# Kernel optimization log

Measured on AMD Instinct MI355X. Metric: run time of the kernel, lower is better.

Reference implementation:

```python
import jax, jax.numpy as jnp
import numpy as np

EPS = 1e-8           # torch.cosine_similarity norm clamp
TEMPERATURE = 0.2    # from __init__ default


def setup_inputs() -> dict:
    key = jax.random.key(0)
    k1, k2, k3 = jax.random.split(key, 3)
    B, C, D = 16384, 1000, 2048  # batch, num_classes, embedding_size
    querys = jax.random.normal(k1, (B, D), dtype=jnp.float32)
    prototype = jax.random.normal(k2, (C, D), dtype=jnp.float32)
    fc_w = jax.random.normal(k3, (C, D), dtype=jnp.float32) * 0.02
    fc_b = jnp.zeros((C,), dtype=jnp.float32)
    return {"querys": querys, "prototype": prototype, "fc_w": fc_w, "fc_b": fc_b}


def _memory_prototype_attention(querys, prototype):
    # cosine similarity of every query against every prototype, fused as one GEMM
    qn = jnp.maximum(jnp.linalg.norm(querys, axis=1, keepdims=True), EPS)      # [B,1]
    pn = jnp.maximum(jnp.linalg.norm(prototype, axis=1, keepdims=True), EPS)   # [C,1]
    cos = jnp.einsum('bd,cd->bc', querys / qn, prototype / pn)                 # [B,C]
    attn = jax.nn.softmax(cos / TEMPERATURE, axis=1)                           # [B,C]
    enhanced = jnp.einsum('bc,cd->bd', attn, prototype)                        # [B,D]
    # original skips rows where the raw score sum is exactly zero
    nonzero = (jnp.sum(cos, axis=1, keepdims=True) != 0)
    return jnp.where(nonzero, enhanced, jnp.zeros_like(enhanced))


def reference(querys, prototype, fc_w, fc_b):
    embedding = querys  # post-avgpool features in the original forward
    enhanced = jax.lax.stop_gradient(_memory_prototype_attention(querys, prototype))
    x = querys + enhanced
    logits = x @ fc_w.T + fc_b  # [B, num_classes]
    return (logits, embedding)
```

## Files before the change

### kernel.cpp

```cpp
#include <hip/hip_runtime.h>
#include <hip/hip_bf16.h>
#include <cstdint>
#include <math.h>

typedef __attribute__((ext_vector_type(8))) __bf16 bfx8;
typedef __attribute__((ext_vector_type(4))) __bf16 bfx4;
typedef __attribute__((ext_vector_type(4))) float f32x4;

#define EPSN 1e-8f
#define SM_SCALE 7.2134752044448170f

__device__ __forceinline__ void gload_lds16(const void* g, void* l) {
    __builtin_amdgcn_global_load_lds(
        (__attribute__((address_space(1))) void*)g,
        (__attribute__((address_space(3))) void*)l,
        16, 0, 0);
}

__global__ __launch_bounds__(256) void qnorm_kernel(
    const float* __restrict__ q, __bf16* __restrict__ qbf,
    float* __restrict__ emb, int D) {
    const int tid = threadIdx.x;
    const size_t roff = (size_t)blockIdx.x * D;
    const float4* qr = (const float4*)(q + roff);
    float4* er = (float4*)(emb + roff);
    const int PASS = D >> 10;
    float4 v[4];
    float ss = 0.f;
    for (int p = 0; p < PASS; ++p) {
        v[p] = qr[p * 256 + tid];
        ss += v[p].x * v[p].x + v[p].y * v[p].y + v[p].z * v[p].z + v[p].w * v[p].w;
    }
    for (int o = 32; o; o >>= 1) ss += __shfl_xor(ss, o);
    __shared__ float sred[4];
    if ((tid & 63) == 0) sred[tid >> 6] = ss;
    __syncthreads();
    float tot = sred[0] + sred[1] + sred[2] + sred[3];
    float inv = 1.f / fmaxf(sqrtf(tot), EPSN);
    for (int p = 0; p < PASS; ++p) {
        er[p * 256 + tid] = v[p];
        bfx4 o4 = {(__bf16)(v[p].x * inv), (__bf16)(v[p].y * inv),
                   (__bf16)(v[p].z * inv), (__bf16)(v[p].w * inv)};
        *(bfx4*)(qbf + roff + (size_t)(p * 256 + tid) * 4) = o4;
    }
}

__global__ __launch_bounds__(256) void pnorm_kernel(
    const float* __restrict__ P, const float* __restrict__ W,
    __bf16* __restrict__ Pn, __bf16* __restrict__ Wb,
    int C, int D) {
    const int c = blockIdx.x;
    const int tid = threadIdx.x;
    const int PASS = D >> 10;
    if (c >= C) {
        bfx4 z = {(__bf16)0.f, (__bf16)0.f, (__bf16)0.f, (__bf16)0.f};
        for (int p = 0; p < PASS; ++p) {
            size_t e = (size_t)c * D + (size_t)(p * 256 + tid) * 4;
            *(bfx4*)(Pn + e) = z;
            *(bfx4*)(Wb + e) = z;
        }
        return;
    }
    const float4* pr = (const float4*)(P + (size_t)c * D);
    float4 v[4];
    float ss = 0.f;
    for (int p = 0; p < PASS; ++p) {
        v[p] = pr[p * 256 + tid];
        ss += v[p].x * v[p].x + v[p].y * v[p].y + v[p].z * v[p].z + v[p].w * v[p].w;
    }
    for (int o = 32; o; o >>= 1) ss += __shfl_xor(ss, o);
    __shared__ float sred[4];
    if ((tid & 63) == 0) sred[tid >> 6] = ss;
    __syncthreads();
    float tot = sred[0] + sred[1] + sred[2] + sred[3];
    float inv = 1.f / fmaxf(sqrtf(tot), EPSN);
    const float4* wr_ = (const float4*)(W + (size_t)c * D);
    for (int p = 0; p < PASS; ++p) {
        size_t e = (size_t)c * D + (size_t)(p * 256 + tid) * 4;
        bfx4 o4 = {(__bf16)(v[p].x * inv), (__bf16)(v[p].y * inv),
                   (__bf16)(v[p].z * inv), (__bf16)(v[p].w * inv)};
        *(bfx4*)(Pn + e) = o4;
        float4 wv = wr_[p * 256 + tid];
        bfx4 w4 = {(__bf16)wv.x, (__bf16)wv.y, (__bf16)wv.z, (__bf16)wv.w};
        *(bfx4*)(Wb + e) = w4;
    }
}

__global__ __launch_bounds__(256) void ptrans_kernel(
    const float* __restrict__ P, __bf16* __restrict__ PT,
    int C, int D, int CP) {
    __shared__ float t[64][65];
    const int d0 = blockIdx.x * 64;
    const int c0 = blockIdx.y * 64;
    const int tid = threadIdx.x;
#pragma unroll
    for (int it = 0; it < 16; ++it) {
        int idx = it * 256 + tid;
        int r = idx >> 6;
        int cc = idx & 63;
        float v = 0.f;
        if (c0 + r < C) v = P[(size_t)(c0 + r) * D + d0 + cc];
        t[r][cc] = v;
    }
    __syncthreads();
#pragma unroll
    for (int it = 0; it < 16; ++it) {
        int idx = it * 256 + tid;
        int dd = idx >> 6;
        int c = idx & 63;
        PT[(size_t)(d0 + dd) * CP + c0 + c] = (__bf16)t[c][dd];
    }
}

__global__ __launch_bounds__(256) void softmax_kernel(
    __bf16* __restrict__ S, int C, int CP) {
    const int tid = threadIdx.x;
    __bf16* row = S + (size_t)blockIdx.x * CP;
    bfx4 v4 = *(const bfx4*)(row + tid * 4);
    const int base = tid * 4;
    float v[4];
    float mx = -INFINITY, rs = 0.f;
#pragma unroll
    for (int j = 0; j < 4; ++j) {
        v[j] = (float)v4[j];
        if (base + j < C) { mx = fmaxf(mx, v[j]); rs += v[j]; }
    }
    for (int o = 32; o; o >>= 1) {
        mx = fmaxf(mx, __shfl_xor(mx, o));
        rs += __shfl_xor(rs, o);
    }
    __shared__ float smx[4], srs[4], sps[4];
    if ((tid & 63) == 0) { smx[tid >> 6] = mx; srs[tid >> 6] = rs; }
    __syncthreads();
    mx = fmaxf(fmaxf(smx[0], smx[1]), fmaxf(smx[2], smx[3]));
    rs = srs[0] + srs[1] + srs[2] + srs[3];
    float p[4], ps = 0.f;
#pragma unroll
    for (int j = 0; j < 4; ++j) {
        p[j] = (base + j < C) ? exp2f((v[j] - mx) * SM_SCALE) : 0.f;
        ps += p[j];
    }
    for (int o = 32; o; o >>= 1) ps += __shfl_xor(ps, o);
    if ((tid & 63) == 0) sps[tid >> 6] = ps;
    __syncthreads();
    ps = sps[0] + sps[1] + sps[2] + sps[3];
    float inv = (rs != 0.f) ? 1.f / ps : 0.f;
    bfx4 o4 = {(__bf16)(p[0] * inv), (__bf16)(p[1] * inv),
               (__bf16)(p[2] * inv), (__bf16)(p[3] * inv)};
    *(bfx4*)(row + tid * 4) = o4;
}

template <int MODE>
__global__ __launch_bounds__(512, 2) void gemm8p(
    const __bf16* __restrict__ A, const __bf16* __restrict__ B_,
    int K, int NT, int nbxl, int nwg,
    void* __restrict__ out, const float* __restrict__ aux, int ldout) {
    __shared__ __bf16 lds[65536];

    const int tid = threadIdx.x;
    const int lane = tid & 63, wid = tid >> 6;
    const int wr = wid >> 2, wc = wid & 3;
    const int fr = lane & 15, fq = lane >> 4;
    const int wr4 = wr * 4, wc2 = wc * 2;
    const int frs = fr * 32 + ((fq * 8) ^ ((fr & 8) << 1));

    const int nbx = 1 << nbxl;
    const int lin = blockIdx.y * nbx + blockIdx.x;
    const int swz = (lin & 7) * (nwg >> 3) + (lin >> 3);
    const int bm0 = (swz >> nbxl) * 256;
    const int bn0 = (swz & (nbx - 1)) * 256;

    int row0, col0, row1, col1;
    {
        int Le = tid * 8;
        int st = Le >> 9, w = Le & 511;
        row0 = (st >> 1) * 16 + (w >> 5);
        col0 = (st & 1) * 32 + ((w & 31) ^ ((w >> 4) & 16));
        Le = tid * 8 + 4096;
        st = Le >> 9; w = Le & 511;
        row1 = (st >> 1) * 16 + (w >> 5);
        col1 = (st & 1) * 32 + ((w & 31) ^ ((w >> 4) & 16));
    }
    const __bf16* Ap = A + (size_t)bm0 * K;
    const __bf16* Bp = B_ + (size_t)bn0 * K;

    auto STAGE = [&](int s) {
        const int t = s >> 2, h = s & 3;
        const int kt = t << 6;
        const int be = ((t & 1) << 14) + ((h >> 1) << 13);
        const __bf16* src = (h & 1) ? Bp : Ap;
        src += (size_t)((h >> 1) * 128) * K + kt;
        __bf16* d = (h & 1) ? (lds + 32768 + be) : (lds + be);
        gload_lds16(src + (size_t)row0 * K + col0, d + tid * 8);
        gload_lds16(src + (size_t)row1 * K + col1, d + tid * 8 + 4096);
    };

    f32x4 acc[4][4][2] = {};

#define PHASE(Q, T, SS, WMODE) do {                                            \
    const int qm_ = (Q) >> 1, qn_ = (Q) & 1;                                   \
    const int bufe_ = ((T) & 1) << 14;                                         \
    bfx8 af_[4][2], bb_[2][2];                                                 \
    _Pragma("unroll") for (int m_ = 0; m_ < 4; ++m_)                           \
      _Pragma("unroll") for (int ks_ = 0; ks_ < 2; ++ks_)                      \
        af_[m_][ks_] = *(const bfx8*)&lds[bufe_ +                              \
            (((qm_ * 8 + wr4 + m_) * 2 + ks_) << 9) + frs];                    \
    _Pragma("unroll") for (int n_ = 0; n_ < 2; ++n_)                           \
      _Pragma("unroll") for (int ks_ = 0; ks_ < 2; ++ks_)                      \
        bb_[n_][ks_] = *(const bfx8*)&lds[32768 + bufe_ +                      \
            (((qn_ * 8 + wc2 + n_) * 2 + ks_) << 9) + frs];                    \
    if ((SS) >= 0) STAGE(SS);                                                  \
    __builtin_amdgcn_s_barrier();                                              \
    asm volatile("s_waitcnt lgkmcnt(0)" ::: "memory");                         \
    __builtin_amdgcn_s_setprio(1);                                             \
    _Pragma("unroll") for (int ks_ = 0; ks_ < 2; ++ks_)                        \
      _Pragma("unroll") for (int m_ = 0; m_ < 4; ++m_)                         \
        _Pragma("unroll") for (int n_ = 0; n_ < 2; ++n_)                       \
          acc[Q][m_][n_] = __builtin_amdgcn_mfma_f32_16x16x32_bf16(            \
              af_[m_][ks_], bb_[n_][ks_], acc[Q][m_][n_], 0, 0, 0);            \
    __builtin_amdgcn_s_setprio(0);                                             \
    if ((WMODE) == 1) asm volatile("s_waitcnt vmcnt(4)" ::: "memory");         \
    else if ((WMODE) == 2) asm volatile("s_waitcnt vmcnt(0)" ::: "memory");    \
    __builtin_amdgcn_s_barrier();                                              \
} while (0)

#pragma unroll
    for (int s = 0; s < 6; ++s) STAGE(s);
    asm volatile("s_waitcnt vmcnt(4)" ::: "memory");
    __builtin_amdgcn_s_barrier();

    int T = 0;
    for (; T <= NT - 3; ++T) {
        PHASE(0, T, 4 * T + 6, 0);
        PHASE(1, T, 4 * T + 7, 0);
        PHASE(2, T, 4 * T + 8, 0);
        PHASE(3, T, 4 * T + 9, 1);
    }
    PHASE(0, T, 4 * T + 6, 0);
    PHASE(1, T, 4 * T + 7, 0);
    PHASE(2, T, -1, 0);
    PHASE(3, T, -1, 2);
    ++T;
    PHASE(0, T, -1, 0);
    PHASE(1, T, -1, 0);
    PHASE(2, T, -1, 0);
    PHASE(3, T, -1, 0);
#undef PHASE

#pragma unroll
    for (int q = 0; q < 4; ++q) {
        const int qm_ = q >> 1, qn_ = q & 1;
#pragma unroll
        for (int m = 0; m < 4; ++m) {
            const int grb = bm0 + qm_ * 128 + wr * 64 + m * 16 + fq * 4;
#pragma unroll
            for (int n = 0; n < 2; ++n) {
                const int gc = bn0 + qn_ * 128 + wc * 32 + n * 16 + fr;
#pragma unroll
                for (int j = 0; j < 4; ++j) {
                    const int gr = grb + j;
                    const float va = acc[q][m][n][j];
                    if (MODE == 0) {
                        ((__bf16*)out)[(size_t)gr * ldout + gc] = (__bf16)va;
                    } else if (MODE == 1) {
                        ((__bf16*)out)[(size_t)gr * ldout + gc] =
                            (__bf16)(va + aux[(size_t)gr * ldout + gc]);
                    } else {
                        if (gc < ldout)
                            ((float*)out)[(size_t)gr * ldout + gc] = va + aux[gc];
                    }
                }
            }
        }
    }
}

extern "C" void kernel_launch(void* const* d_in, const int* in_sizes, int n_in,
                              void* d_out, int out_size, void* d_ws, size_t ws_size,
                              hipStream_t stream) {
    const float* q  = (const float*)d_in[0];
    const float* pr = (const float*)d_in[1];
    const float* fw = (const float*)d_in[2];
    const float* fb = (const float*)d_in[3];
    const int C = in_sizes[3];
    const int D = in_sizes[1] / C;
    const int B = in_sizes[0] / D;
    const int CP = (C + 127) & ~127;

    float* logits = (float*)d_out;
    float* emb = logits + (size_t)B * C;

    char* w = (char*)d_ws;
    __bf16* Qb = (__bf16*)w; w += (size_t)B * D * 2;
    __bf16* Pn = (__bf16*)w; w += (size_t)CP * D * 2;
    __bf16* PT = (__bf16*)w; w += (size_t)D * CP * 2;
    __bf16* Wb = (__bf16*)w; w += (size_t)CP * D * 2;
    __bf16* Sb = (__bf16*)w; w += (size_t)B * CP * 2;
    __bf16* Xb = Qb;

    qnorm_kernel<<<B, 256, 0, stream>>>(q, Qb, emb, D);
    pnorm_kernel<<<CP, 256, 0, stream>>>(pr, fw, Pn, Wb, C, D);
    ptrans_kernel<<<dim3(D / 64, CP / 64), 256, 0, stream>>>(pr, PT, C, D, CP);

    {
        const int nbx = CP / 256, nby = B / 256;
        gemm8p<0><<<dim3(nbx, nby), 512, 0, stream>>>(
            Qb, Pn, D, D / 64, 2, nbx * nby, (void*)Sb, nullptr, CP);
    }
    softmax_kernel<<<B, 256, 0, stream>>>(Sb, C, CP);
    {
        const int nbx = D / 256, nby = B / 256;
        gemm8p<1><<<dim3(nbx, nby), 512, 0, stream>>>(
            Sb, PT, CP, CP / 64, 3, nbx * nby, (void*)Xb, q, D);
    }
    {
        const int nbx = CP / 256, nby = B / 256;
        gemm8p<2><<<dim3(nbx, nby), 512, 0, stream>>>(
            Xb, Wb, D, D / 64, 2, nbx * nby, (void*)logits, fb, C);
    }
}
```

Baseline: 380.3 us.

## Reuse A/B fragments across quadrants and prefetch LDS reads ahead of MFMA

Restructures the GEMM main loop so A and B register fragments are loaded once and reused across two quadrants each (snake order 0,1,3,2), rather than re-reading both for every quadrant. Next-tile fragments are prefetched from LDS while the current MFMAs run, using finer lgkmcnt/vmcnt waits. This cuts LDS read traffic and hides LDS latency behind compute. The cost is more registers for double fragment buffers and delicate waitcnt counts that could be wrong.

```diff
diff --git a/kernel.cpp b/kernel.cpp
--- a/kernel.cpp
+++ b/kernel.cpp
@@ -195,57 +195,81 @@
         gload_lds16(src + (size_t)row1 * K + col1, d + tid * 8 + 4096);
     };
 
+    bfx8 fA0[4][2], fA1[4][2], fB0[2][2], fB1[2][2];
     f32x4 acc[4][4][2] = {};
 
-#define PHASE(Q, T, SS, WMODE) do {                                            \
-    const int qm_ = (Q) >> 1, qn_ = (Q) & 1;                                   \
-    const int bufe_ = ((T) & 1) << 14;                                         \
-    bfx8 af_[4][2], bb_[2][2];                                                 \
+#define RDA(F, H, BUFE) do {                                                   \
     _Pragma("unroll") for (int m_ = 0; m_ < 4; ++m_)                           \
       _Pragma("unroll") for (int ks_ = 0; ks_ < 2; ++ks_)                      \
-        af_[m_][ks_] = *(const bfx8*)&lds[bufe_ +                              \
-            (((qm_ * 8 + wr4 + m_) * 2 + ks_) << 9) + frs];                    \
+        F[m_][ks_] = *(const bfx8*)&lds[(BUFE) +                               \
+            (((((H) * 8) + wr4 + m_) * 2 + ks_) << 9) + frs];                  \
+} while (0)
+#define RDB(F, H, BUFE) do {                                                   \
     _Pragma("unroll") for (int n_ = 0; n_ < 2; ++n_)                           \
       _Pragma("unroll") for (int ks_ = 0; ks_ < 2; ++ks_)                      \
-        bb_[n_][ks_] = *(const bfx8*)&lds[32768 + bufe_ +                      \
-            (((qn_ * 8 + wc2 + n_) * 2 + ks_) << 9) + frs];                    \
-    if ((SS) >= 0) STAGE(SS);                                                  \
-    __builtin_amdgcn_s_barrier();                                              \
-    asm volatile("s_waitcnt lgkmcnt(0)" ::: "memory");                         \
+        F[n_][ks_] = *(const bfx8*)&lds[32768 + (BUFE) +                       \
+            (((((H) * 8) + wc2 + n_) * 2 + ks_) << 9) + frs];                  \
+} while (0)
+#define MM(QI, FA, FB) do {                                                    \
     __builtin_amdgcn_s_setprio(1);                                             \
     _Pragma("unroll") for (int ks_ = 0; ks_ < 2; ++ks_)                        \
       _Pragma("unroll") for (int m_ = 0; m_ < 4; ++m_)                         \
         _Pragma("unroll") for (int n_ = 0; n_ < 2; ++n_)                       \
-          acc[Q][m_][n_] = __builtin_amdgcn_mfma_f32_16x16x32_bf16(            \
-              af_[m_][ks_], bb_[n_][ks_], acc[Q][m_][n_], 0, 0, 0);            \
+          acc[QI][m_][n_] = __builtin_amdgcn_mfma_f32_16x16x32_bf16(           \
+              FA[m_][ks_], FB[n_][ks_], acc[QI][m_][n_], 0, 0, 0);             \
     __builtin_amdgcn_s_setprio(0);                                             \
-    if ((WMODE) == 1) asm volatile("s_waitcnt vmcnt(4)" ::: "memory");         \
-    else if ((WMODE) == 2) asm volatile("s_waitcnt vmcnt(0)" ::: "memory");    \
-    __builtin_amdgcn_s_barrier();                                              \
 } while (0)
+#define BAR __builtin_amdgcn_s_barrier()
+#define LGKM(N) asm volatile("s_waitcnt lgkmcnt(" #N ")" ::: "memory")
+#define VMC(N) asm volatile("s_waitcnt vmcnt(" #N ")" ::: "memory")
 
 #pragma unroll
     for (int s = 0; s < 6; ++s) STAGE(s);
-    asm volatile("s_waitcnt vmcnt(4)" ::: "memory");
-    __builtin_amdgcn_s_barrier();
-
-    int T = 0;
-    for (; T <= NT - 3; ++T) {
-        PHASE(0, T, 4 * T + 6, 0);
-        PHASE(1, T, 4 * T + 7, 0);
-        PHASE(2, T, 4 * T + 8, 0);
-        PHASE(3, T, 4 * T + 9, 1);
-    }
-    PHASE(0, T, 4 * T + 6, 0);
-    PHASE(1, T, 4 * T + 7, 0);
-    PHASE(2, T, -1, 0);
-    PHASE(3, T, -1, 2);
-    ++T;
-    PHASE(0, T, -1, 0);
-    PHASE(1, T, -1, 0);
-    PHASE(2, T, -1, 0);
-    PHASE(3, T, -1, 0);
-#undef PHASE
+    VMC(4);
+    BAR;
+    RDA(fA0, 0, 0);
+    RDB(fB0, 0, 0);
+
+    for (int T = 0; T <= NT - 3; ++T) {
+        const int bufe = (T & 1) << 14, nbufe = bufe ^ 16384;
+        RDB(fB1, 1, bufe); STAGE(4 * T + 6); BAR; LGKM(4);
+        MM(0, fA0, fB0); BAR;
+        RDA(fA1, 1, bufe); STAGE(4 * T + 7); BAR; LGKM(8);
+        MM(1, fA0, fB1); VMC(6); BAR;
+        RDA(fA0, 0, nbufe); STAGE(4 * T + 8); BAR; LGKM(8);
+        MM(3, fA1, fB1); VMC(6); BAR;
+        STAGE(4 * T + 9); BAR; LGKM(8);
+        MM(2, fA1, fB0); RDB(fB0, 0, nbufe); VMC(4); BAR;
+    }
+    {
+        const int T = NT - 2;
+        const int bufe = (T & 1) << 14, nbufe = bufe ^ 16384;
+        RDB(fB1, 1, bufe); STAGE(4 * T + 6); BAR; LGKM(4);
+        MM(0, fA0, fB0); BAR;
+        RDA(fA1, 1, bufe); STAGE(4 * T + 7); BAR; LGKM(8);
+        MM(1, fA0, fB1); VMC(6); BAR;
+        RDA(fA0, 0, nbufe); BAR; LGKM(8);
+        MM(3, fA1, fB1); VMC(4); BAR;
+        BAR; LGKM(8);
+        MM(2, fA1, fB0); RDB(fB0, 0, nbufe); VMC(0); BAR;
+    }
+    {
+        const int T = NT - 1;
+        const int bufe = (T & 1) << 14;
+        RDB(fB1, 1, bufe); BAR; LGKM(4);
+        MM(0, fA0, fB0); BAR;
+        RDA(fA1, 1, bufe); BAR; LGKM(8);
+        MM(1, fA0, fB1); BAR;
+        BAR; LGKM(0);
+        MM(3, fA1, fB1); BAR;
+        MM(2, fA1, fB0);
+    }
+#undef RDA
+#undef RDB
+#undef MM
+#undef BAR
+#undef LGKM
+#undef VMC
 
 #pragma unroll
     for (int q = 0; q < 4; ++q) {
```

Result: no change. 387.1 us (+1.8%).
